# Performance work log

Hardware: AMD Instinct MI355X
Metric: run time of the kernel (lower is better)

Reference implementation:

```python
import jax, jax.numpy as jnp
import numpy as np

IN_F = 8192
OUT_F = 8192
R = 16
LORA_ALPHA = 32
BLOCK = 64
SCALING = LORA_ALPHA / R  # 2.0
NUMEL = IN_F * OUT_F


def dequantize_4bit(packed, scales):
    # packed: [numel//2] bytes (stored as int32 in [0,255]); element 2i = low nibble, 2i+1 = high nibble
    low = packed & 0xF
    high = (packed >> 4) & 0xF
    q = jnp.stack([low, high], axis=-1).reshape(-1)          # [numel] ints in [0,15]
    flat = q.astype(jnp.float32) - 8.0                        # signed 4-bit
    flat = (flat.reshape(-1, BLOCK) * scales[:, None]).reshape(-1)  # blockwise scale
    return flat.reshape(OUT_F, IN_F)


def setup_inputs() -> dict:
    key = jax.random.key(0)
    k1, k2, k3, k4, k5 = jax.random.split(key, 5)
    x = jax.random.normal(k1, (1, 64, IN_F), dtype=jnp.float32)
    packed_weights = jax.random.randint(k2, (NUMEL // 2,), 0, 256, dtype=jnp.int32)
    block_scales = jax.random.uniform(k3, (NUMEL // BLOCK,), dtype=jnp.float32) * 0.05
    # kaiming_uniform(a=sqrt(5)) on [R, IN_F] -> bound = 1/sqrt(IN_F)
    bound = 1.0 / np.sqrt(IN_F)
    lora_A = jax.random.uniform(k4, (R, IN_F), minval=-bound, maxval=bound, dtype=jnp.float32)
    # original init is zeros; use small randn for a non-trivial baseline
    lora_B = jax.random.normal(k5, (OUT_F, R), dtype=jnp.float32) * 0.02
    return {"x": x, "packed_weights": packed_weights, "block_scales": block_scales,
            "lora_A": lora_A, "lora_B": lora_B}


def reference(x, packed_weights, block_scales, lora_A, lora_B):
    W = dequantize_4bit(packed_weights, block_scales).astype(x.dtype)  # [OUT_F, IN_F]
    base_out = jnp.einsum('bsi,oi->bso', x, W)                         # no bias (bias_buffer=None)
    lora_out = jnp.einsum('bsr,or->bso', jnp.einsum('bsi,ri->bsr', x, lora_A), lora_B) * SCALING
    return base_out + lora_out
```

## Files before the change

kernel.cpp:

```cpp
#include <hip/hip_runtime.h>
#include <hip/hip_bf16.h>

#define IN_F 8192
#define OUT_F 8192
#define SEQ 64
#define LORA_R 16
#define KH 4096

typedef __attribute__((ext_vector_type(4))) float f32x4;
typedef __attribute__((ext_vector_type(4))) int i32x4;
typedef __attribute__((ext_vector_type(8))) unsigned short u16x8;
typedef __attribute__((ext_vector_type(4))) unsigned short u16x4;
typedef _Float16 f16x2 __attribute__((ext_vector_type(2)));
typedef _Float16 f16x8 __attribute__((ext_vector_type(8)));

typedef __attribute__((address_space(3))) unsigned int lds_u32;
typedef const __attribute__((address_space(1))) unsigned int glb_u32;

__device__ __forceinline__ void gl_lds16(const void* g, void* l) {
    __builtin_amdgcn_global_load_lds((glb_u32*)g, (lds_u32*)l, 16, 0, 0);
}

__global__ __launch_bounds__(256) void k_prep(
    const float* __restrict__ x, const float* __restrict__ A,
    unsigned short* __restrict__ xb, float* __restrict__ t) {
    __shared__ float part[64];
    const int s = blockIdx.x;
    const int w = threadIdx.x >> 6, lane = threadIdx.x & 63;
    const int kbase = w * 2048;
    const float* xr = x + s * IN_F + kbase;

    f32x4 xv[8];
    #pragma unroll
    for (int j = 0; j < 8; ++j) {
        xv[j] = *(const f32x4*)(xr + j * 256 + lane * 4);
        u16x4 h;
        h[0] = __builtin_bit_cast(unsigned short, (_Float16)xv[j].x);
        h[1] = __builtin_bit_cast(unsigned short, (_Float16)xv[j].y);
        h[2] = __builtin_bit_cast(unsigned short, (_Float16)xv[j].z);
        h[3] = __builtin_bit_cast(unsigned short, (_Float16)xv[j].w);
        *(u16x4*)(xb + s * IN_F + kbase + j * 256 + lane * 4) = h;
    }

    float acc[LORA_R];
    #pragma unroll
    for (int r = 0; r < LORA_R; ++r) acc[r] = 0.f;
    #pragma unroll
    for (int r = 0; r < LORA_R; ++r) {
        const float* ar = A + r * IN_F + kbase;
        #pragma unroll
        for (int j = 0; j < 8; ++j) {
            f32x4 av = *(const f32x4*)(ar + j * 256 + lane * 4);
            acc[r] = fmaf(xv[j].x, av.x, acc[r]);
            acc[r] = fmaf(xv[j].y, av.y, acc[r]);
            acc[r] = fmaf(xv[j].z, av.z, acc[r]);
            acc[r] = fmaf(xv[j].w, av.w, acc[r]);
        }
    }
    #pragma unroll
    for (int r = 0; r < LORA_R; ++r) {
        float v = acc[r];
        #pragma unroll
        for (int off = 32; off; off >>= 1) v += __shfl_down(v, off, 64);
        if (lane == 0) part[w * 16 + r] = v;
    }
    __syncthreads();
    if (threadIdx.x < 16)
        t[s * LORA_R + threadIdx.x] = part[threadIdx.x] + part[16 + threadIdx.x] +
                                      part[32 + threadIdx.x] + part[48 + threadIdx.x];
}

__global__ __launch_bounds__(512, 4) void k_main(
    const int* __restrict__ packed, const float* __restrict__ scales,
    const unsigned short* __restrict__ xb, const float* __restrict__ t,
    const float* __restrict__ B, float* __restrict__ out) {
    __shared__ char lds[57856];
    _Float16* xs = (_Float16*)lds;
    int* wt = (int*)(lds + 32768);
    float* scs = (float*)(lds + 49152);
    float* accs = (float*)lds;

    const int tid = threadIdx.x;
    const int n0 = (blockIdx.x >> 1) * 32;
    const int kh = blockIdx.x & 1;
    const int w = tid >> 6, lane = tid & 63;
    const int nh = w >> 2, wkk = w & 3;
    const int q = lane >> 4, c16 = lane & 15;

    const int lrow = lane >> 4, lcol = lane & 15;
    const int xr0 = w * 8 + lrow, xr1 = xr0 + 4;
    const int wr  = w * 4 + lrow;
    const unsigned short* xg0 = xb + (size_t)xr0 * IN_F + kh * KH + ((lcol ^ (xr0 & 7)) << 3);
    const unsigned short* xg1 = xb + (size_t)xr1 * IN_F + kh * KH + ((lcol ^ (xr1 & 7)) << 3);
    const int* wgp = packed + (long)(n0 + wr) * (IN_F / 2) + kh * (KH / 2) + ((lcol ^ (wr & 7)) << 2);

    _Float16* xd0 = xs + w * 8 * 128;
    _Float16* xd1 = xd0 + 4 * 128;
    int* wd = wt + w * 256;

    {
        int row = tid >> 4, g = tid & 15;
        f32x4 v = *(const f32x4*)(scales + (n0 + row) * (IN_F / 64) + kh * 64 + g * 4);
        *(f32x4*)(scs + row * 68 + g * 4) = v;
    }

    f32x4 acc[4];
    #pragma unroll
    for (int mt = 0; mt < 4; ++mt) acc[mt] = (f32x4){0.f, 0.f, 0.f, 0.f};

    const int pvo = (nh * 16 + c16) * 64 + ((wkk * 16 + q * 4) ^ ((c16 & 7) << 2));
    int afo[4];
    #pragma unroll
    for (int mt = 0; mt < 4; ++mt)
        afo[mt] = (mt * 16 + c16) * 128 + ((wkk * 32 + q * 8) ^ ((c16 & 7) << 3));
    const int sco = (nh * 16 + c16) * 68 + (wkk >> 1);

    gl_lds16(xg0, xd0);
    gl_lds16(xg1, xd1);
    gl_lds16(wgp, wd);

    const f16x2 c1032 = {(_Float16)1032.0f, (_Float16)1032.0f};

    for (int kt = 0; kt < 32; ++kt) {
        asm volatile("s_waitcnt vmcnt(0) lgkmcnt(0)" ::: "memory");
        __builtin_amdgcn_s_barrier();
        __builtin_amdgcn_sched_barrier(0);
        const int cur = kt & 1;
        if (kt < 31) {
            const int nb = 1 - cur;
            const size_t xoff = (size_t)(kt + 1) * 128;
            gl_lds16(xg0 + xoff, xd0 + nb * 8192);
            gl_lds16(xg1 + xoff, xd1 + nb * 8192);
            gl_lds16(wgp + (kt + 1) * 64, wd + nb * 2048);
        }
        i32x4 pv = *(const i32x4*)(wt + cur * 2048 + pvo);
        float scf = scs[sco + kt * 2];
        _Float16 sch = (_Float16)scf;
        f16x2 sc2 = {sch, sch};
        f16x8 bf;
        #pragma unroll
        for (int m = 0; m < 4; ++m) {
            unsigned u = ((((unsigned)pv[m] << 12) | (unsigned)pv[m]) & 0x000F000Fu) | 0x64006400u;
            f16x2 h = __builtin_bit_cast(f16x2, u);
            h = (h - c1032) * sc2;
            bf[2 * m] = h.x;
            bf[2 * m + 1] = h.y;
        }
        const _Float16* xbase = xs + cur * 8192;
        #pragma unroll
        for (int mt = 0; mt < 4; ++mt) {
            f16x8 af = *(const f16x8*)(xbase + afo[mt]);
            acc[mt] = __builtin_amdgcn_mfma_f32_16x16x32_f16(af, bf, acc[mt], 0, 0, 0);
        }
    }
    __syncthreads();

    float* myacc = accs + w * (64 * 17);
    #pragma unroll
    for (int mt = 0; mt < 4; ++mt)
        #pragma unroll
        for (int r = 0; r < 4; ++r)
            myacc[(mt * 16 + q * 4 + r) * 17 + c16] = acc[mt][r];
    __syncthreads();

    #pragma unroll
    for (int j = 0; j < 4; ++j) {
        int p = tid + j * 512;
        int s = p >> 5, c = p & 31;
        const float* ab = accs + (c >> 4) * 4 * (64 * 17) + s * 17 + (c & 15);
        float v = ab[0] + ab[64 * 17] + ab[2 * 64 * 17] + ab[3 * 64 * 17];
        if (kh == 0) {
            const float* tp = t + s * LORA_R;
            const float* bp = B + (n0 + c) * LORA_R;
            f32x4 t0 = *(const f32x4*)tp,       t1 = *(const f32x4*)(tp + 4);
            f32x4 t2 = *(const f32x4*)(tp + 8), t3 = *(const f32x4*)(tp + 12);
            f32x4 b0 = *(const f32x4*)bp,       b1 = *(const f32x4*)(bp + 4);
            f32x4 b2 = *(const f32x4*)(bp + 8), b3 = *(const f32x4*)(bp + 12);
            float lr = t0.x * b0.x + t0.y * b0.y + t0.z * b0.z + t0.w * b0.w
                     + t1.x * b1.x + t1.y * b1.y + t1.z * b1.z + t1.w * b1.w
                     + t2.x * b2.x + t2.y * b2.y + t2.z * b2.z + t2.w * b2.w
                     + t3.x * b3.x + t3.y * b3.y + t3.z * b3.z + t3.w * b3.w;
            v += 2.0f * lr;
        }
        unsafeAtomicAdd(&out[s * OUT_F + n0 + c], v);
    }
}

extern "C" void kernel_launch(void* const* d_in, const int* in_sizes, int n_in,
                              void* d_out, int out_size, void* d_ws, size_t ws_size,
                              hipStream_t stream) {
    const float* x      = (const float*)d_in[0];
    const int* packed   = (const int*)d_in[1];
    const float* scales = (const float*)d_in[2];
    const float* lora_A = (const float*)d_in[3];
    const float* lora_B = (const float*)d_in[4];
    float* out = (float*)d_out;

    unsigned short* xb = (unsigned short*)d_ws;
    float* t = (float*)((char*)d_ws + (size_t)SEQ * IN_F * 2);

    hipMemsetAsync(out, 0, (size_t)SEQ * OUT_F * sizeof(float), stream);
    k_prep<<<SEQ, 256, 0, stream>>>(x, lora_A, xb, t);
    k_main<<<512, 512, 0, stream>>>(packed, scales, xb, t, lora_B, out);
}
```

Before: 233.1 us.

## Drop split-K atomics, use full-K blocks with triple-buffered prefetch

The main kernel no longer splits K across two blocks. Each of 256 blocks now covers the full K range, so the output memset and the atomic adds are replaced by plain stores. The LDS pipeline goes from double to triple buffering with a partial vmcnt wait, keeping two tiles in flight, and the LDS footprint grows so occupancy drops to 2 blocks per CU. The prep kernel is split across twice as many blocks, and the LoRA partial sums are merged in the epilogue. The risk is that 256 blocks fill fewer CUs than the previous 512.

```diff
diff --git a/kernel.cpp b/kernel.cpp
--- a/kernel.cpp
+++ b/kernel.cpp
@@ -5,7 +5,6 @@
 #define OUT_F 8192
 #define SEQ 64
 #define LORA_R 16
-#define KH 4096
 
 typedef __attribute__((ext_vector_type(4))) float f32x4;
 typedef __attribute__((ext_vector_type(4))) int i32x4;
@@ -25,14 +24,14 @@
     const float* __restrict__ x, const float* __restrict__ A,
     unsigned short* __restrict__ xb, float* __restrict__ t) {
     __shared__ float part[64];
-    const int s = blockIdx.x;
+    const int s = blockIdx.x >> 1, p = blockIdx.x & 1;
     const int w = threadIdx.x >> 6, lane = threadIdx.x & 63;
-    const int kbase = w * 2048;
+    const int kbase = p * 4096 + w * 1024;
     const float* xr = x + s * IN_F + kbase;
 
-    f32x4 xv[8];
-    #pragma unroll
-    for (int j = 0; j < 8; ++j) {
+    f32x4 xv[4];
+    #pragma unroll
+    for (int j = 0; j < 4; ++j) {
         xv[j] = *(const f32x4*)(xr + j * 256 + lane * 4);
         u16x4 h;
         h[0] = __builtin_bit_cast(unsigned short, (_Float16)xv[j].x);
@@ -49,7 +48,7 @@
     for (int r = 0; r < LORA_R; ++r) {
         const float* ar = A + r * IN_F + kbase;
         #pragma unroll
-        for (int j = 0; j < 8; ++j) {
+        for (int j = 0; j < 4; ++j) {
             f32x4 av = *(const f32x4*)(ar + j * 256 + lane * 4);
             acc[r] = fmaf(xv[j].x, av.x, acc[r]);
             acc[r] = fmaf(xv[j].y, av.y, acc[r]);
@@ -66,23 +65,22 @@
     }
     __syncthreads();
     if (threadIdx.x < 16)
-        t[s * LORA_R + threadIdx.x] = part[threadIdx.x] + part[16 + threadIdx.x] +
-                                      part[32 + threadIdx.x] + part[48 + threadIdx.x];
-}
-
-__global__ __launch_bounds__(512, 4) void k_main(
+        t[s * 32 + p * 16 + threadIdx.x] = part[threadIdx.x] + part[16 + threadIdx.x] +
+                                           part[32 + threadIdx.x] + part[48 + threadIdx.x];
+}
+
+__global__ __launch_bounds__(512, 2) void k_main(
     const int* __restrict__ packed, const float* __restrict__ scales,
     const unsigned short* __restrict__ xb, const float* __restrict__ t,
     const float* __restrict__ B, float* __restrict__ out) {
-    __shared__ char lds[57856];
+    __shared__ char lds[90624];
     _Float16* xs = (_Float16*)lds;
-    int* wt = (int*)(lds + 32768);
-    float* scs = (float*)(lds + 49152);
+    int* wt = (int*)(lds + 49152);
+    float* scs = (float*)(lds + 73728);
     float* accs = (float*)lds;
 
     const int tid = threadIdx.x;
-    const int n0 = (blockIdx.x >> 1) * 32;
-    const int kh = blockIdx.x & 1;
+    const int n0 = blockIdx.x * 32;
     const int w = tid >> 6, lane = tid & 63;
     const int nh = w >> 2, wkk = w & 3;
     const int q = lane >> 4, c16 = lane & 15;
@@ -90,9 +88,9 @@
     const int lrow = lane >> 4, lcol = lane & 15;
     const int xr0 = w * 8 + lrow, xr1 = xr0 + 4;
     const int wr  = w * 4 + lrow;
-    const unsigned short* xg0 = xb + (size_t)xr0 * IN_F + kh * KH + ((lcol ^ (xr0 & 7)) << 3);
-    const unsigned short* xg1 = xb + (size_t)xr1 * IN_F + kh * KH + ((lcol ^ (xr1 & 7)) << 3);
-    const int* wgp = packed + (long)(n0 + wr) * (IN_F / 2) + kh * (KH / 2) + ((lcol ^ (wr & 7)) << 2);
+    const unsigned short* xg0 = xb + (size_t)xr0 * IN_F + ((lcol ^ (xr0 & 7)) << 3);
+    const unsigned short* xg1 = xb + (size_t)xr1 * IN_F + ((lcol ^ (xr1 & 7)) << 3);
+    const int* wgp = packed + (long)(n0 + wr) * (IN_F / 2) + ((lcol ^ (wr & 7)) << 2);
 
     _Float16* xd0 = xs + w * 8 * 128;
     _Float16* xd1 = xd0 + 4 * 128;
@@ -100,8 +98,9 @@
 
     {
         int row = tid >> 4, g = tid & 15;
-        f32x4 v = *(const f32x4*)(scales + (n0 + row) * (IN_F / 64) + kh * 64 + g * 4);
-        *(f32x4*)(scs + row * 68 + g * 4) = v;
+        const float* sp = scales + (n0 + row) * (IN_F / 64);
+        *(f32x4*)(scs + row * 132 + g * 4)      = *(const f32x4*)(sp + g * 4);
+        *(f32x4*)(scs + row * 132 + 64 + g * 4) = *(const f32x4*)(sp + 64 + g * 4);
     }
 
     f32x4 acc[4];
@@ -113,25 +112,31 @@
     #pragma unroll
     for (int mt = 0; mt < 4; ++mt)
         afo[mt] = (mt * 16 + c16) * 128 + ((wkk * 32 + q * 8) ^ ((c16 & 7) << 3));
-    const int sco = (nh * 16 + c16) * 68 + (wkk >> 1);
+    const int sco = (nh * 16 + c16) * 132 + (wkk >> 1);
+
+    asm volatile("s_waitcnt lgkmcnt(0)" ::: "memory");
+    __builtin_amdgcn_s_barrier();
 
     gl_lds16(xg0, xd0);
     gl_lds16(xg1, xd1);
     gl_lds16(wgp, wd);
+    gl_lds16(xg0 + 128, xd0 + 8192);
+    gl_lds16(xg1 + 128, xd1 + 8192);
+    gl_lds16(wgp + 64,  wd + 2048);
 
     const f16x2 c1032 = {(_Float16)1032.0f, (_Float16)1032.0f};
 
-    for (int kt = 0; kt < 32; ++kt) {
-        asm volatile("s_waitcnt vmcnt(0) lgkmcnt(0)" ::: "memory");
+    int cur = 0, nxt = 2;
+    for (int kt = 0; kt < 64; ++kt) {
+        if (kt < 63) asm volatile("s_waitcnt vmcnt(3)" ::: "memory");
+        else         asm volatile("s_waitcnt vmcnt(0)" ::: "memory");
         __builtin_amdgcn_s_barrier();
         __builtin_amdgcn_sched_barrier(0);
-        const int cur = kt & 1;
-        if (kt < 31) {
-            const int nb = 1 - cur;
-            const size_t xoff = (size_t)(kt + 1) * 128;
-            gl_lds16(xg0 + xoff, xd0 + nb * 8192);
-            gl_lds16(xg1 + xoff, xd1 + nb * 8192);
-            gl_lds16(wgp + (kt + 1) * 64, wd + nb * 2048);
+        if (kt < 62) {
+            const size_t xoff = (size_t)(kt + 2) * 128;
+            gl_lds16(xg0 + xoff, xd0 + nxt * 8192);
+            gl_lds16(xg1 + xoff, xd1 + nxt * 8192);
+            gl_lds16(wgp + (kt + 2) * 64, wd + nxt * 2048);
         }
         i32x4 pv = *(const i32x4*)(wt + cur * 2048 + pvo);
         float scf = scs[sco + kt * 2];
@@ -152,6 +157,8 @@
             f16x8 af = *(const f16x8*)(xbase + afo[mt]);
             acc[mt] = __builtin_amdgcn_mfma_f32_16x16x32_f16(af, bf, acc[mt], 0, 0, 0);
         }
+        cur = (cur == 2) ? 0 : cur + 1;
+        nxt = (nxt == 2) ? 0 : nxt + 1;
     }
     __syncthreads();
 
@@ -169,20 +176,20 @@
         int s = p >> 5, c = p & 31;
         const float* ab = accs + (c >> 4) * 4 * (64 * 17) + s * 17 + (c & 15);
         float v = ab[0] + ab[64 * 17] + ab[2 * 64 * 17] + ab[3 * 64 * 17];
-        if (kh == 0) {
-            const float* tp = t + s * LORA_R;
-            const float* bp = B + (n0 + c) * LORA_R;
-            f32x4 t0 = *(const f32x4*)tp,       t1 = *(const f32x4*)(tp + 4);
-            f32x4 t2 = *(const f32x4*)(tp + 8), t3 = *(const f32x4*)(tp + 12);
-            f32x4 b0 = *(const f32x4*)bp,       b1 = *(const f32x4*)(bp + 4);
-            f32x4 b2 = *(const f32x4*)(bp + 8), b3 = *(const f32x4*)(bp + 12);
-            float lr = t0.x * b0.x + t0.y * b0.y + t0.z * b0.z + t0.w * b0.w
-                     + t1.x * b1.x + t1.y * b1.y + t1.z * b1.z + t1.w * b1.w
-                     + t2.x * b2.x + t2.y * b2.y + t2.z * b2.z + t2.w * b2.w
-                     + t3.x * b3.x + t3.y * b3.y + t3.z * b3.z + t3.w * b3.w;
-            v += 2.0f * lr;
-        }
-        unsafeAtomicAdd(&out[s * OUT_F + n0 + c], v);
+        const float* tp = t + s * 32;
+        const float* bp = B + (n0 + c) * LORA_R;
+        f32x4 t0 = *(const f32x4*)tp        + *(const f32x4*)(tp + 16);
+        f32x4 t1 = *(const f32x4*)(tp + 4)  + *(const f32x4*)(tp + 20);
+        f32x4 t2 = *(const f32x4*)(tp + 8)  + *(const f32x4*)(tp + 24);
+        f32x4 t3 = *(const f32x4*)(tp + 12) + *(const f32x4*)(tp + 28);
+        f32x4 b0 = *(const f32x4*)bp,       b1 = *(const f32x4*)(bp + 4);
+        f32x4 b2 = *(const f32x4*)(bp + 8), b3 = *(const f32x4*)(bp + 12);
+        float lr = t0.x * b0.x + t0.y * b0.y + t0.z * b0.z + t0.w * b0.w
+                 + t1.x * b1.x + t1.y * b1.y + t1.z * b1.z + t1.w * b1.w
+                 + t2.x * b2.x + t2.y * b2.y + t2.z * b2.z + t2.w * b2.w
+                 + t3.x * b3.x + t3.y * b3.y + t3.z * b3.z + t3.w * b3.w;
+        v += 2.0f * lr;
+        out[s * OUT_F + n0 + c] = v;
     }
 }
 
@@ -199,7 +206,6 @@
     unsigned short* xb = (unsigned short*)d_ws;
     float* t = (float*)((char*)d_ws + (size_t)SEQ * IN_F * 2);
 
-    hipMemsetAsync(out, 0, (size_t)SEQ * OUT_F * sizeof(float), stream);
-    k_prep<<<SEQ, 256, 0, stream>>>(x, lora_A, xb, t);
-    k_main<<<512, 512, 0, stream>>>(packed, scales, xb, t, lora_B, out);
-}
+    k_prep<<<128, 256, 0, stream>>>(x, lora_A, xb, t);
+    k_main<<<256, 512, 0, stream>>>(packed, scales, xb, t, lora_B, out);
+}
```

Result: faster. 221.0 us (-5.2%).
